# Kernel optimization log

Hardware: AMD Instinct MI355X
Metric: run time of the kernel (lower is better)

Reference implementation:

```python
import math
import jax, jax.numpy as jnp
import numpy as np

NUM_HEADS = 16
HEAD_DIM = 64
NB_FEATURES = 256
EPS = 1e-06
DATA_NORM = HEAD_DIM ** (-0.25)


def setup_inputs() -> dict:
    key = jax.random.key(0)
    ks = jax.random.split(key, 5)
    B, N, C = 4, 4096, 1024
    x = jax.random.normal(ks[0], (B, N, C), dtype=jnp.float32)
    w_qkv = jax.random.normal(ks[1], (C, 3 * C), dtype=jnp.float32) * (C ** -0.5)
    b_qkv = jnp.zeros((3 * C,), dtype=jnp.float32)
    w_out = jax.random.normal(ks[2], (C, C), dtype=jnp.float32) * (C ** -0.5)
    b_out = jnp.zeros((C,), dtype=jnp.float32)
    proj = jax.random.normal(ks[3], (NUM_HEADS, NB_FEATURES, HEAD_DIM), dtype=jnp.float32)
    proj = proj / jnp.linalg.norm(proj, axis=-1, keepdims=True)  # F.normalize(dim=-1)
    return {"x": x, "w_qkv": w_qkv, "b_qkv": b_qkv, "w_out": w_out, "b_out": b_out,
            "proj_matrix": proj}


def _feature_map(x, proj):
    # x: [b,h,n,d], proj: [h,m,d] -> [b,h,n,m]
    x = x * DATA_NORM
    x_proj = jnp.einsum('bhnd,hmd->bhnm', x, proj)
    sq_norms = 0.5 * jnp.sum(x * x, axis=-1, keepdims=True)
    x_proj = x_proj - sq_norms
    x_proj = x_proj - jnp.max(x_proj, axis=-1, keepdims=True)
    return (jnp.exp(x_proj) + EPS) / math.sqrt(NB_FEATURES)


def reference(x, w_qkv, b_qkv, w_out, b_out, proj_matrix):
    B, N, C = x.shape
    h, d = NUM_HEADS, HEAD_DIM
    qkv = x @ w_qkv + b_qkv                     # [B,N,3C]
    q, k, v = jnp.split(qkv, 3, axis=-1)
    to_heads = lambda z: z.reshape(B, N, h, d).transpose(0, 2, 1, 3)  # [B,h,N,d]
    q, k, v = to_heads(q), to_heads(k), to_heads(v)

    q_prime = _feature_map(q, proj_matrix)      # [B,h,N,m]
    k_prime = _feature_map(k, proj_matrix)      # [B,h,N,m]

    k_sum = jnp.sum(k_prime, axis=2)                          # [B,h,m]
    kv = jnp.einsum('bhnm,bhnd->bhmd', k_prime, v)            # [B,h,m,d]
    numerator = jnp.einsum('bhnm,bhmd->bhnd', q_prime, kv)    # [B,h,N,d]
    denominator = jnp.einsum('bhnm,bhm->bhn', q_prime, k_sum) + EPS
    out = numerator / denominator[..., None]

    out = out.transpose(0, 2, 1, 3).reshape(B, N, C)
    return out @ w_out + b_out
```

## Files before the change

### kernel.cpp

```cpp
#include <hip/hip_runtime.h>
#include <hip/hip_bf16.h>
#include <stdint.h>


#define DN 0.35355339059327379f
#define EPSF 1e-6f
#define INV_SQRT_M 0.0625f

typedef __attribute__((ext_vector_type(8))) short bf16x8;
typedef __attribute__((ext_vector_type(4))) float f32x4;

static __device__ __forceinline__ short f2bf(float f) {
    __hip_bfloat16 h = __float2bfloat16(f);
    return *(short*)&h;
}
static __device__ __forceinline__ void gload16(const void* g, void* l) {
    __builtin_amdgcn_global_load_lds(
        (const __attribute__((address_space(1))) void*)g,
        (__attribute__((address_space(3))) void*)l,
        16, 0, 0);
}

__global__ __launch_bounds__(256) void conv_x(const float* __restrict__ X,
                                              short* __restrict__ Xb) {
    int i = blockIdx.x * 256 + threadIdx.x;
    float4 v = ((const float4*)X)[i];
    short4 o;
    o.x = f2bf(v.x); o.y = f2bf(v.y); o.z = f2bf(v.z); o.w = f2bf(v.w);
    ((short4*)Xb)[i] = o;
}

__global__ __launch_bounds__(256) void convt_w(const float* __restrict__ W,
                                               short* __restrict__ WT,
                                               int K, int NN) {
    __shared__ short tile[64][66];
    int t = threadIdx.x;
    int k0 = blockIdx.y * 64, n0 = blockIdx.x * 64;
    for (int i = t; i < 4096; i += 256) {
        int r = i >> 6, c = i & 63;
        tile[r][c] = f2bf(W[(size_t)(k0 + r) * NN + n0 + c]);
    }
    __syncthreads();
    for (int i = t; i < 4096; i += 256) {
        int r = i >> 6, c = i & 63;
        WT[(size_t)(n0 + r) * K + k0 + c] = tile[c][r];
    }
}

__global__ __launch_bounds__(256) void conv_proj(const float* __restrict__ proj,
                                                 short* __restrict__ pjb) {
    int e = blockIdx.x * 256 + threadIdx.x;
    int m = (e >> 6) & 255, d = e & 63;
    int base = e & ~63;
    pjb[base + (d ^ ((m & 7) << 3))] = f2bf(proj[e]);
}

__device__ __forceinline__ void gemm_core128(const short* __restrict__ A,
                                             const short* __restrict__ BT,
                                             int rowBase, int colBase,
                                             char* smem, f32x4 acc[4][4]) {
    const int K = 1024;
    int t = threadIdx.x, lane = t & 63, w = t >> 6;
    int li = lane & 15, g = lane >> 4;
    int wm = w >> 1, wn = w & 1;

    const char* aSrc[4]; const char* bSrc[4]; int aOff[4];
#pragma unroll
    for (int c = 0; c < 4; ++c) {
        int idx = c * 256 + t;
        int r = idx >> 3, s = t & 7;
        aOff[c] = idx * 16;
        aSrc[c] = (const char*)(A + (size_t)(rowBase + r) * K + ((s ^ (r & 7)) * 8));
        bSrc[c] = (const char*)(BT + (size_t)(colBase + r) * K + ((s ^ (r & 7)) * 8));
    }
#pragma unroll
    for (int m = 0; m < 4; ++m)
#pragma unroll
        for (int n = 0; n < 4; ++n) acc[m][n] = (f32x4){0.f, 0.f, 0.f, 0.f};

#pragma unroll
    for (int c = 0; c < 4; ++c) {
        gload16(aSrc[c], smem + aOff[c]);
        gload16(bSrc[c], smem + 16384 + aOff[c]);
    }

    int swz = (li & 7) << 4;

    for (int tt = 0; tt < 16; ++tt) {
        int cur = tt & 1;
        if (tt < 15) {
            char* d = smem + (cur ^ 1) * 32768;
#pragma unroll
            for (int c = 0; c < 4; ++c) {
                gload16(aSrc[c] + (size_t)(tt + 1) * 128, d + aOff[c]);
                gload16(bSrc[c] + (size_t)(tt + 1) * 128, d + 16384 + aOff[c]);
            }
            asm volatile("s_waitcnt vmcnt(8)" ::: "memory");
        } else {
            asm volatile("s_waitcnt vmcnt(0)" ::: "memory");
        }
        __builtin_amdgcn_sched_barrier(0);
        __builtin_amdgcn_s_barrier();
        __builtin_amdgcn_sched_barrier(0);
        __builtin_amdgcn_s_setprio(1);
        const char* bA = smem + cur * 32768;
        const char* bB = bA + 16384;
#pragma unroll
        for (int ks = 0; ks < 2; ++ks) {
            int kb = ks * 64 + g * 16;
            bf16x8 af[4], bv[4];
#pragma unroll
            for (int m = 0; m < 4; ++m)
                af[m] = *(const bf16x8*)(bA + (wm * 64 + m * 16 + li) * 128 + (kb ^ swz));
#pragma unroll
            for (int n = 0; n < 4; ++n)
                bv[n] = *(const bf16x8*)(bB + (wn * 64 + n * 16 + li) * 128 + (kb ^ swz));
#pragma unroll
            for (int m = 0; m < 4; ++m)
#pragma unroll
                for (int n = 0; n < 4; ++n)
                    acc[m][n] = __builtin_amdgcn_mfma_f32_16x16x32_bf16(
                        af[m], bv[n], acc[m][n], 0, 0, 0);
        }
        __builtin_amdgcn_s_setprio(0);
        __builtin_amdgcn_sched_barrier(0);
        __builtin_amdgcn_s_barrier();
        __builtin_amdgcn_sched_barrier(0);
    }
}

__global__ __launch_bounds__(256, 2) void mfma_gemm_qkv(
        const short* __restrict__ A, const short* __restrict__ BT,
        const float* __restrict__ bias,
        short* __restrict__ Qh, short* __restrict__ Kh, short* __restrict__ Vt) {
    __shared__ __align__(16) char smem[65536];
    int t = threadIdx.x, lane = t & 63, w = t >> 6;
    int li = lane & 15, g = lane >> 4, wm = w >> 1, wn = w & 1;
    int lin = blockIdx.x;
    int bx = lin % 24, by = lin / 24;
    int rowBase = by * 128, colBase = bx * 128;

    f32x4 acc[4][4];
    gemm_core128(A, BT, rowBase, colBase, smem, acc);

    float bcol[4];
#pragma unroll
    for (int n = 0; n < 4; ++n) bcol[n] = bias[colBase + wn * 64 + n * 16 + li];
    int whichB = colBase >> 10;

    if (whichB == 2) {
#pragma unroll
        for (int n = 0; n < 4; ++n) {
            int gc = colBase + wn * 64 + n * 16 + li;
            int hh = (gc & 1023) >> 6, dd = gc & 63;
#pragma unroll
            for (int m = 0; m < 4; ++m) {
                int gr0 = rowBase + wm * 64 + m * 16 + g * 4;
                int b = gr0 >> 12, nn0 = gr0 & 4095;
                short4 o;
                o.x = f2bf(acc[m][n][0] + bcol[n]);
                o.y = f2bf(acc[m][n][1] + bcol[n]);
                o.z = f2bf(acc[m][n][2] + bcol[n]);
                o.w = f2bf(acc[m][n][3] + bcol[n]);
                int nsw = (nn0 & ~63) | ((nn0 & 63) ^ ((dd & 7) << 3));
                *(short4*)&Vt[((size_t)(b * 16 + hh) * 64 + dd) * 4096 + nsw] = o;
            }
        }
    } else {
        short* dst = (whichB == 0) ? Qh : Kh;
        int hh = ((colBase + wn * 64) & 1023) >> 6;
        float* wreg = (float*)(smem + w * 8704);
#pragma unroll
        for (int r = 0; r < 2; ++r) {
#pragma unroll
            for (int mi = 0; mi < 2; ++mi)
#pragma unroll
                for (int n = 0; n < 4; ++n)
#pragma unroll
                    for (int jj = 0; jj < 4; ++jj)
                        wreg[(mi * 16 + g * 4 + jj) * 68 + n * 16 + li] =
                            (acc[2 * r + mi][n][jj] + bcol[n]) * DN;
            int row = lane >> 1, h2 = lane & 1;
            int tok = rowBase + wm * 64 + r * 32 + row;
            int b = tok >> 12, nn = tok & 4095;
            size_t base = ((size_t)(b * 16 + hh) * 4096 + nn) * 64;
#pragma unroll
            for (int k = 0; k < 4; ++k) {
                float4 v0 = *(const float4*)&wreg[row * 68 + h2 * 32 + k * 8];
                float4 v1 = *(const float4*)&wreg[row * 68 + h2 * 32 + k * 8 + 4];
                bf16x8 ov;
                ov[0] = f2bf(v0.x); ov[1] = f2bf(v0.y);
                ov[2] = f2bf(v0.z); ov[3] = f2bf(v0.w);
                ov[4] = f2bf(v1.x); ov[5] = f2bf(v1.y);
                ov[6] = f2bf(v1.z); ov[7] = f2bf(v1.w);
                int dgrp = (h2 * 4 + k) ^ (tok & 7);
                *(bf16x8*)&dst[base + dgrp * 8] = ov;
            }
        }
    }
}

template<int Q, int S>
static __device__ __forceinline__ void phase_compute(
        const char* smem, int tt, int wm, int wn, int li, int g, int swz,
        f32x4 (&acc)[2][4][2][2]) {
    const char* bA = smem + ((tt & 1) << 16) + (Q << 14);
    const char* bB = smem + ((tt & 1) << 16) + 32768 + (S << 14);
    bf16x8 af[4][2], bf[2][2];
#pragma unroll
    for (int fr = 0; fr < 4; ++fr) {
        int row = wm * 64 + fr * 16 + li;
#pragma unroll
        for (int kk = 0; kk < 2; ++kk)
            af[fr][kk] = *(const bf16x8*)(bA + row * 128 + ((kk * 64 + g * 16) ^ swz));
    }
#pragma unroll
    for (int fn = 0; fn < 2; ++fn) {
        int row = wn * 32 + fn * 16 + li;
#pragma unroll
        for (int kk = 0; kk < 2; ++kk)
            bf[fn][kk] = *(const bf16x8*)(bB + row * 128 + ((kk * 64 + g * 16) ^ swz));
    }
    __builtin_amdgcn_s_setprio(1);
#pragma unroll
    for (int kk = 0; kk < 2; ++kk)
#pragma unroll
        for (int fr = 0; fr < 4; ++fr)
#pragma unroll
            for (int fn = 0; fn < 2; ++fn)
                acc[Q][fr][S][fn] = __builtin_amdgcn_mfma_f32_16x16x32_bf16(
                    af[fr][kk], bf[fn][kk], acc[Q][fr][S][fn], 0, 0, 0);
    __builtin_amdgcn_s_setprio(0);
}

static __device__ __forceinline__ void gemm_core256(const short* __restrict__ A,
                                                    const short* __restrict__ BT,
                                                    int rowBase, int colBase,
                                                    char* smem,
                                                    f32x4 (&acc)[2][4][2][2]) {
    const int K = 1024;
    int t = threadIdx.x, lane = t & 63;
    int li = lane & 15, g = lane >> 4;
    int w = t >> 6, wm = w >> 2, wn = w & 3;
    int swz = (li & 7) << 4;

    int idxA = t, idxB = 512 + t;
    int rA = idxA >> 3, sA = idxA & 7;
    int rB = idxB >> 3, sB = idxB & 7;
    const char* Ab = (const char*)(A + (size_t)rowBase * K);
    const char* Bb = (const char*)(BT + (size_t)colBase * K);
    int srcOffA = rA * 2048 + ((sA ^ (rA & 7)) * 16);
    int srcOffB = rB * 2048 + ((sB ^ (rB & 7)) * 16);
    int dstOffA = idxA * 16, dstOffB = idxB * 16;

#define STG(op_, half_, tile_) do {                                           \
    char* d_ = smem + (((tile_) & 1) << 16) + ((op_) << 15) + ((half_) << 14);\
    const char* s_ = ((op_) ? Bb : Ab) + (half_) * 262144 + (tile_) * 128;    \
    gload16(s_ + srcOffA, d_ + dstOffA);                                      \
    gload16(s_ + srcOffB, d_ + dstOffB);                                      \
} while (0)

#define PH(q_, s_, vm_, dost_, sop_, shalf_, stile_) do {                     \
    if (dost_) STG(sop_, shalf_, stile_);                                     \
    asm volatile("s_waitcnt vmcnt(" #vm_ ")" ::: "memory");                   \
    __builtin_amdgcn_sched_barrier(0);                                        \
    __builtin_amdgcn_s_barrier();                                             \
    __builtin_amdgcn_sched_barrier(0);                                        \
    phase_compute<q_, s_>(smem, tt, wm, wn, li, g, swz, acc);                 \
} while (0)

#pragma unroll
    for (int q = 0; q < 2; ++q)
#pragma unroll
        for (int fr = 0; fr < 4; ++fr)
#pragma unroll
            for (int s = 0; s < 2; ++s)
#pragma unroll
                for (int fn = 0; fn < 2; ++fn)
                    acc[q][fr][s][fn] = (f32x4){0.f, 0.f, 0.f, 0.f};

    STG(1, 0, 0);
    STG(0, 1, 0);
    STG(0, 0, 0);
    STG(1, 1, 0);
    STG(1, 0, 1);
    STG(0, 1, 1);

    for (int tt = 0; tt < 14; ++tt) {
        PH(0, 0,  8, true, 0, 0, tt + 1);
        PH(1, 0, 12, true, 1, 1, tt + 1);
        PH(1, 1, 10, true, 1, 0, tt + 2);
        PH(0, 1, 12, true, 0, 1, tt + 2);
    }
    {
        int tt = 14;
        PH(0, 0,  8, true, 0, 0, 15);
        PH(1, 0, 12, true, 1, 1, 15);
        PH(1, 1,  8, false, 0, 0, 0);
        PH(0, 1,  8, false, 0, 0, 0);
    }
    {
        int tt = 15;
        PH(0, 0, 2, false, 0, 0, 0);
        PH(1, 0, 4, false, 0, 0, 0);
        PH(1, 1, 0, false, 0, 0, 0);
        PH(0, 1, 0, false, 0, 0, 0);
    }
    __builtin_amdgcn_s_barrier();
#undef PH
#undef STG
}

__global__ __launch_bounds__(512) void mfma_gemm_out(
        const short* __restrict__ A, const short* __restrict__ BT,
        const float* __restrict__ bias, float* __restrict__ C) {
    __shared__ __align__(16) char smem[131072];
    int lin = blockIdx.x;
    int bx = lin & 3, by = lin >> 2;
    int rowBase = by * 256, colBase = bx * 256;

    f32x4 acc[2][4][2][2];
    gemm_core256(A, BT, rowBase, colBase, smem, acc);

    int t = threadIdx.x, lane = t & 63, w = t >> 6;
    int li = lane & 15, g = lane >> 4, wm = w >> 2, wn = w & 3;
    float bcol[2][2];
#pragma unroll
    for (int s = 0; s < 2; ++s)
#pragma unroll
        for (int fn = 0; fn < 2; ++fn)
            bcol[s][fn] = bias[colBase + s * 128 + wn * 32 + fn * 16 + li];

    float* wreg = (float*)(smem + w * 5632);
#pragma unroll
    for (int q = 0; q < 2; ++q)
#pragma unroll
        for (int fp = 0; fp < 2; ++fp)
#pragma unroll
            for (int s = 0; s < 2; ++s) {
#pragma unroll
                for (int fr2 = 0; fr2 < 2; ++fr2)
#pragma unroll
                    for (int fn = 0; fn < 2; ++fn)
#pragma unroll
                        for (int jj = 0; jj < 4; ++jj)
                            wreg[(fr2 * 16 + g * 4 + jj) * 44 + fn * 16 + li] =
                                acc[q][fp * 2 + fr2][s][fn][jj] + bcol[s][fn];
                int row2 = lane >> 1, hh2 = lane & 1;
                int gr = rowBase + q * 128 + wm * 64 + fp * 32 + row2;
                float* cp = C + (size_t)gr * 1024 + colBase + s * 128 + wn * 32 + hh2 * 16;
#pragma unroll
                for (int k = 0; k < 4; ++k)
                    *(float4*)&cp[k * 4] = *(const float4*)&wreg[row2 * 44 + hh2 * 16 + k * 4];
            }
}

__global__ __launch_bounds__(256) void fmap_mfma(const short* __restrict__ Kh,
                                                 const short* __restrict__ Vt,
                                                 const short* __restrict__ pjb,
                                                 float* __restrict__ kvpart,
                                                 float* __restrict__ kspart) {
    int bh = blockIdx.y, ch = blockIdx.x, h = bh & 15;
    int t = threadIdx.x, lane = t & 63, w = t >> 6;
    int g = lane >> 4, li = lane & 15;
    __shared__ __align__(16) short pj[256 * 64];
    __shared__ __align__(16) short kt[64 * 64];
    __shared__ __align__(16) short vt[64 * 64];
    __shared__ __align__(16) short Pl[4][64 * 40];
    __shared__ __align__(16) float maxw[4][64];

    const short* kbase = Kh + ((size_t)bh * 4096 + ch * 512) * 64;
    const short* vbase = Vt + (size_t)bh * 64 * 4096 + ch * 512;

    {
        const short* psrc = pjb + (size_t)h * 16384;
#pragma unroll
        for (int c2 = 0; c2 < 8; ++c2) {
            int c = 8 * w + c2;
            gload16(psrc + c * 512 + lane * 8, pj + c * 512);
        }
#pragma unroll
        for (int c2 = 0; c2 < 2; ++c2) {
            int c = 2 * w + c2;
            gload16(kbase + c * 512 + lane * 8, kt + c * 512);
            int d = 8 * c + (lane >> 3);
            gload16(vbase + (size_t)d * 4096 + (lane & 7) * 8, vt + c * 512);
        }
    }
    __syncthreads();

    f32x4 acc[4][4];
#pragma unroll
    for (int i = 0; i < 4; ++i)
#pragma unroll
        for (int j = 0; j < 4; ++j) acc[i][j] = (f32x4){0.f, 0.f, 0.f, 0.f};
    float ksacc[4] = {0.f, 0.f, 0.f, 0.f};

    int swz = (li & 7) << 4;

    for (int tile = 0; tile < 8; ++tile) {
        bf16x8 rk0, rk1, rv0, rv1;
        if (tile < 7) {
            int c0 = 2 * w, c1 = 2 * w + 1;
            size_t kof = (size_t)((tile + 1) * 64) * 64;
            rk0 = *(const bf16x8*)(kbase + kof + c0 * 512 + lane * 8);
            rk1 = *(const bf16x8*)(kbase + kof + c1 * 512 + lane * 8);
            int d0 = 8 * c0 + (lane >> 3), d1 = 8 * c1 + (lane >> 3);
            rv0 = *(const bf16x8*)(vbase + (size_t)d0 * 4096 + (tile + 1) * 64 + (lane & 7) * 8);
            rv1 = *(const bf16x8*)(vbase + (size_t)d1 * 4096 + (tile + 1) * 64 + (lane & 7) * 8);
        }

        f32x4 sacc[4][4];
#pragma unroll
        for (int i = 0; i < 4; ++i)
#pragma unroll
            for (int j = 0; j < 4; ++j) sacc[i][j] = (f32x4){0.f, 0.f, 0.f, 0.f};
#pragma unroll
        for (int ks = 0; ks < 2; ++ks) {
            int kb = ks * 64 + g * 16;
            bf16x8 afr[4], bfr[4];
#pragma unroll
            for (int ni = 0; ni < 4; ++ni)
                afr[ni] = *(const bf16x8*)((const char*)kt +
                           (16 * ni + li) * 128 + (kb ^ swz));
#pragma unroll
            for (int mi = 0; mi < 4; ++mi)
                bfr[mi] = *(const bf16x8*)((const char*)pj +
                           (64 * w + 16 * mi + li) * 128 + (kb ^ swz));
#pragma unroll
            for (int ni = 0; ni < 4; ++ni)
#pragma unroll
                for (int mi = 0; mi < 4; ++mi)
                    sacc[ni][mi] = __builtin_amdgcn_mfma_f32_16x16x32_bf16(
                        afr[ni], bfr[mi], sacc[ni][mi], 0, 0, 0);
        }

        float mxl[4][4];
#pragma unroll
        for (int ni = 0; ni < 4; ++ni)
#pragma unroll
            for (int jj = 0; jj < 4; ++jj) {
                float m0 = fmaxf(sacc[ni][0][jj], sacc[ni][1][jj]);
                float m1 = fmaxf(sacc[ni][2][jj], sacc[ni][3][jj]);
                mxl[ni][jj] = fmaxf(m0, m1);
            }
#pragma unroll
        for (int off = 1; off <= 8; off <<= 1)
#pragma unroll
            for (int ni = 0; ni < 4; ++ni)
#pragma unroll
                for (int jj = 0; jj < 4; ++jj)
                    mxl[ni][jj] = fmaxf(mxl[ni][jj], __shfl_xor(mxl[ni][jj], off));
        if (li == 0) {
#pragma unroll
            for (int ni = 0; ni < 4; ++ni)
                *(float4*)&maxw[w][16 * ni + 4 * g] =
                    make_float4(mxl[ni][0], mxl[ni][1], mxl[ni][2], mxl[ni][3]);
        }
        __syncthreads();

#pragma unroll
        for (int hf = 0; hf < 2; ++hf) {
#pragma unroll
            for (int ni2 = 0; ni2 < 2; ++ni2) {
                int ni = 2 * hf + ni2;
                float4 a0 = *(const float4*)&maxw[0][16 * ni + 4 * g];
                float4 a1 = *(const float4*)&maxw[1][16 * ni + 4 * g];
                float4 a2 = *(const float4*)&maxw[2][16 * ni + 4 * g];
                float4 a3 = *(const float4*)&maxw[3][16 * ni + 4 * g];
                float mm[4];
                mm[0] = fmaxf(fmaxf(a0.x, a1.x), fmaxf(a2.x, a3.x));
                mm[1] = fmaxf(fmaxf(a0.y, a1.y), fmaxf(a2.y, a3.y));
                mm[2] = fmaxf(fmaxf(a0.z, a1.z), fmaxf(a2.z, a3.z));
                mm[3] = fmaxf(fmaxf(a0.w, a1.w), fmaxf(a2.w, a3.w));
#pragma unroll
                for (int mi = 0; mi < 4; ++mi) {
                    float p0 = (__expf(sacc[ni][mi][0] - mm[0]) + EPSF) * INV_SQRT_M;
                    float p1 = (__expf(sacc[ni][mi][1] - mm[1]) + EPSF) * INV_SQRT_M;
                    float p2 = (__expf(sacc[ni][mi][2] - mm[2]) + EPSF) * INV_SQRT_M;
                    float p3 = (__expf(sacc[ni][mi][3] - mm[3]) + EPSF) * INV_SQRT_M;
                    ksacc[mi] += (p0 + p1) + (p2 + p3);
                    uint32_t u0 = (uint32_t)(uint16_t)f2bf(p0) |
                                  ((uint32_t)(uint16_t)f2bf(p1) << 16);
                    uint32_t u1 = (uint32_t)(uint16_t)f2bf(p2) |
                                  ((uint32_t)(uint16_t)f2bf(p3) << 16);
                    int m_l = 16 * mi + li;
                    *(uint2*)((char*)Pl[w] + m_l * 80 + 32 * ni2 + 8 * g) =
                        make_uint2(u0, u1);
                }
            }
#pragma unroll
            for (int mi = 0; mi < 4; ++mi) {
                bf16x8 pa = *(const bf16x8*)((const char*)Pl[w] +
                             (16 * mi + li) * 80 + 16 * g);
#pragma unroll
                for (int di = 0; di < 4; ++di) {
                    bf16x8 bv = *(const bf16x8*)((const char*)vt +
                                 (16 * di + li) * 128 + ((64 * hf + 16 * g) ^ swz));
                    acc[mi][di] = __builtin_amdgcn_mfma_f32_16x16x32_bf16(
                        pa, bv, acc[mi][di], 0, 0, 0);
                }
            }
        }
        __syncthreads();
        if (tile < 7) {
            int c0 = 2 * w, c1 = 2 * w + 1;
            *(bf16x8*)((char*)kt + c0 * 1024 + lane * 16) = rk0;
            *(bf16x8*)((char*)kt + c1 * 1024 + lane * 16) = rk1;
            *(bf16x8*)((char*)vt + c0 * 1024 + lane * 16) = rv0;
            *(bf16x8*)((char*)vt + c1 * 1024 + lane * 16) = rv1;
            __syncthreads();
        }
    }

#pragma unroll
    for (int mi = 0; mi < 4; ++mi) {
        ksacc[mi] += __shfl_xor(ksacc[mi], 16);
        ksacc[mi] += __shfl_xor(ksacc[mi], 32);
    }
    if (lane < 16) {
#pragma unroll
        for (int mi = 0; mi < 4; ++mi)
            kspart[(bh * 8 + ch) * 256 + 64 * w + 16 * mi + li] = ksacc[mi];
    }
    float* kvb = kvpart + (size_t)(bh * 8 + ch) * 16384;
#pragma unroll
    for (int mi = 0; mi < 4; ++mi)
#pragma unroll
        for (int di = 0; di < 4; ++di) {
            int d = 16 * di + li, m0 = 64 * w + 16 * mi + 4 * g;
            *(float4*)&kvb[d * 256 + m0] =
                make_float4(acc[mi][di][0], acc[mi][di][1],
                            acc[mi][di][2], acc[mi][di][3]);
        }
}

__global__ __launch_bounds__(256) void reduce_kv(const float* __restrict__ kvpart,
                                                 const float* __restrict__ kspart,
                                                 short* __restrict__ kvsT) {
    int bh = blockIdx.y, bx = blockIdx.x, t = threadIdx.x;
    if (bx < 4) {
#pragma unroll
        for (int i = 0; i < 16; ++i) {
            int idx = t + i * 256;
            int d = 16 * bx + (idx >> 8), m = idx & 255;
            float s = 0.f;
            size_t base = ((size_t)(bh * 8) * 64 + d) * 256 + m;
#pragma unroll
            for (int c = 0; c < 8; ++c) s += kvpart[base + (size_t)c * 16384];
            int widx = (m & 128) + ((m & 127) ^ ((d & 7) << 3));
            kvsT[((size_t)bh * 80 + d) * 256 + widx] = f2bf(s);
        }
    } else {
        float s = 0.f;
#pragma unroll
        for (int c = 0; c < 8; ++c) s += kspart[((bh * 8 + c) << 8) + t];
        kvsT[((size_t)bh * 80 + 64) * 256 + t] = f2bf(s);
        for (int i = t; i < 15 * 256; i += 256) {
            int r = 65 + (i >> 8), cc = i & 255;
            kvsT[((size_t)bh * 80 + r) * 256 + cc] = 0;
        }
    }
}

__global__ __launch_bounds__(256) void contract_mfma(
        const short* __restrict__ Qh,
        const short* __restrict__ pjb,
        const short* __restrict__ kvsT,
        short* __restrict__ attn) {
    int bh = blockIdx.y, rb = blockIdx.x, h = bh & 15, b = bh >> 4;
    int t = threadIdx.x, lane = t & 63, w = t >> 6;
    __shared__ __align__(16) short qs[128 * 64];
    __shared__ __align__(16) short pj[128 * 64];
    __shared__ __align__(16) short Pl[64 * 128];
    __shared__ __align__(16) short kvl[80 * 128];

    {
        const short* src = Qh + ((size_t)bh * 4096 + rb * 128) * 64;
#pragma unroll
        for (int c2 = 0; c2 < 4; ++c2) {
            int c = 4 * w + c2;
            gload16(src + (c * 8 + (lane >> 3)) * 64 + (lane & 7) * 8,
                    qs + c * 512);
        }
    }

    f32x4 acc5[2][5];
#pragma unroll
    for (int rg = 0; rg < 2; ++rg)
#pragma unroll
        for (int i = 0; i < 5; ++i) acc5[rg][i] = (f32x4){0.f, 0.f, 0.f, 0.f};

    int g = lane >> 4, li = lane & 15;

    for (int half = 0; half < 2; ++half) {
        const short* psrc = pjb + (size_t)h * 16384 + half * 8192;
#pragma unroll
        for (int c2 = 0; c2 < 4; ++c2) {
            int c = 4 * w + c2;
            gload16(psrc + (c * 8 + (lane >> 3)) * 64 + (lane & 7) * 8,
                    pj + c * 512);
        }
        const short* ksrc = kvsT + (size_t)bh * 80 * 256 + half * 128;
#pragma unroll
        for (int c2 = 0; c2 < 5; ++c2) {
            int c = 5 * w + c2;
            gload16(ksrc + (c * 4 + (lane >> 4)) * 256 + (lane & 15) * 8,
                    kvl + c * 512);
        }
        __syncthreads();

#pragma unroll
        for (int rg = 0; rg < 2; ++rg) {
            f32x4 sacc[2][4];
#pragma unroll
            for (int mi = 0; mi < 2; ++mi)
#pragma unroll
                for (int ni = 0; ni < 4; ++ni) sacc[mi][ni] = (f32x4){0.f, 0.f, 0.f, 0.f};
#pragma unroll
            for (int ks = 0; ks < 2; ++ks) {
                int kbyte = ks * 64 + g * 16;
                bf16x8 afr[2], bfr[4];
#pragma unroll
                for (int mi = 0; mi < 2; ++mi) {
                    int mr = 32 * w + 16 * mi + li;
                    afr[mi] = *(const bf16x8*)((const char*)pj +
                               mr * 128 + (kbyte ^ ((mr & 7) << 4)));
                }
#pragma unroll
                for (int ni = 0; ni < 4; ++ni) {
                    int qr = rg * 64 + 16 * ni + li;
                    bfr[ni] = *(const bf16x8*)((const char*)qs +
                               qr * 128 + (kbyte ^ ((qr & 7) << 4)));
                }
#pragma unroll
                for (int mi = 0; mi < 2; ++mi)
#pragma unroll
                    for (int ni = 0; ni < 4; ++ni)
                        sacc[mi][ni] = __builtin_amdgcn_mfma_f32_16x16x32_bf16(
                            afr[mi], bfr[ni], sacc[mi][ni], 0, 0, 0);
            }

#pragma unroll
            for (int mi = 0; mi < 2; ++mi) {
                int m0 = 32 * w + 16 * mi + 4 * g;
#pragma unroll
                for (int ni = 0; ni < 4; ++ni) {
                    int row = 16 * ni + li;
                    float e0 = (__expf(sacc[mi][ni][0]) + EPSF) * INV_SQRT_M;
                    float e1 = (__expf(sacc[mi][ni][1]) + EPSF) * INV_SQRT_M;
                    float e2 = (__expf(sacc[mi][ni][2]) + EPSF) * INV_SQRT_M;
                    float e3 = (__expf(sacc[mi][ni][3]) + EPSF) * INV_SQRT_M;
                    uint32_t u0 = (uint32_t)(uint16_t)f2bf(e0) |
                                  ((uint32_t)(uint16_t)f2bf(e1) << 16);
                    uint32_t u1 = (uint32_t)(uint16_t)f2bf(e2) |
                                  ((uint32_t)(uint16_t)f2bf(e3) << 16);
                    int byte = row * 256 + ((m0 * 2) ^ ((row & 7) << 4));
                    *(uint2*)((char*)Pl + byte) = make_uint2(u0, u1);
                }
            }
            __syncthreads();

            int rowA = 16 * w + li;
            int abase = rowA * 256;
            int asw = (rowA & 7) << 4;
#pragma unroll
            for (int ks = 0; ks < 4; ++ks) {
                int kbyte = ks * 64 + g * 16;
                bf16x8 pa = *(const bf16x8*)((const char*)Pl + abase + (kbyte ^ asw));
#pragma unroll
                for (int ni = 0; ni < 5; ++ni) {
                    int rowB = 16 * ni + li;
                    bf16x8 bv = *(const bf16x8*)((const char*)kvl +
                                 rowB * 256 + (kbyte ^ ((rowB & 7) << 4)));
                    acc5[rg][ni] = __builtin_amdgcn_mfma_f32_16x16x32_bf16(
                        pa, bv, acc5[rg][ni], 0, 0, 0);
                }
            }
            __syncthreads();
        }
    }

#pragma unroll
    for (int rg = 0; rg < 2; ++rg) {
        float dj[4];
#pragma unroll
        for (int jj = 0; jj < 4; ++jj)
            dj[jj] = __shfl(acc5[rg][4][jj], lane & 48) + EPSF;
#pragma unroll
        for (int ni = 0; ni < 4; ++ni) {
            int d = 16 * ni + li;
#pragma unroll
            for (int jj = 0; jj < 4; ++jj) {
                int n = rb * 128 + rg * 64 + 16 * w + 4 * g + jj;
                attn[((size_t)b * 4096 + n) * 1024 + h * 64 + d] =
                    f2bf(acc5[rg][ni][jj] / dj[jj]);
            }
        }
    }
}

extern "C" void kernel_launch(void* const* d_in, const int* in_sizes, int n_in,
                              void* d_out, int out_size, void* d_ws, size_t ws_size,
                              hipStream_t stream) {
    const float* x      = (const float*)d_in[0];
    const float* w_qkv  = (const float*)d_in[1];
    const float* b_qkv  = (const float*)d_in[2];
    const float* w_out  = (const float*)d_in[3];
    const float* b_out  = (const float*)d_in[4];
    const float* proj   = (const float*)d_in[5];
    float* out = (float*)d_out;

    char* w = (char*)d_ws;
    short* xb     = (short*)(w);
    short* wqT    = (short*)(w + 33554432);
    short* wOT    = (short*)(w + 39845888);
    short* Qh     = (short*)(w + 41943040);
    short* Kh     = (short*)(w + 75497472);
    short* Vt     = (short*)(w + 109051904);
    float* kvpart = (float*)(w);
    float* kspart = (float*)(w + 142606336);
    short* kvsT   = (short*)(w + 143130624);
    short* pjb    = (short*)(w + 145752064);
    short* attn   = Kh;

    conv_x<<<dim3(16384), 256, 0, stream>>>(x, xb);
    convt_w<<<dim3(48, 16), 256, 0, stream>>>(w_qkv, wqT, 1024, 3072);
    convt_w<<<dim3(16, 16), 256, 0, stream>>>(w_out, wOT, 1024, 1024);
    conv_proj<<<dim3(1024), 256, 0, stream>>>(proj, pjb);
    mfma_gemm_qkv<<<dim3(3072), 256, 0, stream>>>(xb, wqT, b_qkv, Qh, Kh, Vt);
    fmap_mfma<<<dim3(8, 64), 256, 0, stream>>>(Kh, Vt, pjb, kvpart, kspart);
    reduce_kv<<<dim3(5, 64), 256, 0, stream>>>(kvpart, kspart, kvsT);
    contract_mfma<<<dim3(32, 64), 256, 0, stream>>>(Qh, pjb, kvsT, attn);
    mfma_gemm_out<<<dim3(256), 512, 0, stream>>>(attn, wOT, b_out, out);
}
```

Measured before the change: 308.6 us.

## Merge prep conversion kernels into one launch and keep projection fragments in registers

Folds the four input-conversion kernels (x to bf16, both weight transposes, projection swizzle) into one kernel that branches on block index, cutting three launches and the gaps between them. In fmap_mfma and contract_mfma the projection matrix is no longer staged in shared memory. Each wave loads its fixed projection MFMA fragments straight from global memory into registers once and reuses them across tiles. This drops shared-memory traffic and LDS footprint, which may raise occupancy, but it adds register pressure and uncoalesced fragment loads.

New measurement: 298.6 us. -3.2%, faster.

```diff
diff --git a/kernel.cpp b/kernel.cpp
--- a/kernel.cpp
+++ b/kernel.cpp
@@ -21,38 +21,54 @@
         16, 0, 0);
 }
 
-__global__ __launch_bounds__(256) void conv_x(const float* __restrict__ X,
-                                              short* __restrict__ Xb) {
-    int i = blockIdx.x * 256 + threadIdx.x;
-    float4 v = ((const float4*)X)[i];
-    short4 o;
-    o.x = f2bf(v.x); o.y = f2bf(v.y); o.z = f2bf(v.z); o.w = f2bf(v.w);
-    ((short4*)Xb)[i] = o;
-}
-
-__global__ __launch_bounds__(256) void convt_w(const float* __restrict__ W,
-                                               short* __restrict__ WT,
-                                               int K, int NN) {
+__global__ __launch_bounds__(256) void prep(const float* __restrict__ X,
+                                            short* __restrict__ Xb,
+                                            const float* __restrict__ Wq,
+                                            short* __restrict__ WqT,
+                                            const float* __restrict__ Wo,
+                                            short* __restrict__ WoT,
+                                            const float* __restrict__ proj,
+                                            short* __restrict__ pjb) {
     __shared__ short tile[64][66];
-    int t = threadIdx.x;
-    int k0 = blockIdx.y * 64, n0 = blockIdx.x * 64;
-    for (int i = t; i < 4096; i += 256) {
-        int r = i >> 6, c = i & 63;
-        tile[r][c] = f2bf(W[(size_t)(k0 + r) * NN + n0 + c]);
-    }
-    __syncthreads();
-    for (int i = t; i < 4096; i += 256) {
-        int r = i >> 6, c = i & 63;
-        WT[(size_t)(n0 + r) * K + k0 + c] = tile[c][r];
-    }
-}
-
-__global__ __launch_bounds__(256) void conv_proj(const float* __restrict__ proj,
-                                                 short* __restrict__ pjb) {
-    int e = blockIdx.x * 256 + threadIdx.x;
-    int m = (e >> 6) & 255, d = e & 63;
-    int base = e & ~63;
-    pjb[base + (d ^ ((m & 7) << 3))] = f2bf(proj[e]);
+    int b = blockIdx.x, t = threadIdx.x;
+    if (b < 16384) {
+        int i = b * 256 + t;
+        float4 v = ((const float4*)X)[i];
+        short4 o;
+        o.x = f2bf(v.x); o.y = f2bf(v.y); o.z = f2bf(v.z); o.w = f2bf(v.w);
+        ((short4*)Xb)[i] = o;
+    } else if (b < 17152) {
+        int idx = b - 16384;
+        int k0 = (idx / 48) * 64, n0 = (idx % 48) * 64;
+        const int K = 1024, NN = 3072;
+        for (int i = t; i < 4096; i += 256) {
+            int r = i >> 6, c = i & 63;
+            tile[r][c] = f2bf(Wq[(size_t)(k0 + r) * NN + n0 + c]);
+        }
+        __syncthreads();
+        for (int i = t; i < 4096; i += 256) {
+            int r = i >> 6, c = i & 63;
+            WqT[(size_t)(n0 + r) * K + k0 + c] = tile[c][r];
+        }
+    } else if (b < 17408) {
+        int idx = b - 17152;
+        int k0 = (idx / 16) * 64, n0 = (idx % 16) * 64;
+        const int K = 1024, NN = 1024;
+        for (int i = t; i < 4096; i += 256) {
+            int r = i >> 6, c = i & 63;
+            tile[r][c] = f2bf(Wo[(size_t)(k0 + r) * NN + n0 + c]);
+        }
+        __syncthreads();
+        for (int i = t; i < 4096; i += 256) {
+            int r = i >> 6, c = i & 63;
+            WoT[(size_t)(n0 + r) * K + k0 + c] = tile[c][r];
+        }
+    } else {
+        int e = (b - 17408) * 256 + t;
+        int m = (e >> 6) & 255, d = e & 63;
+        int base = e & ~63;
+        pjb[base + (d ^ ((m & 7) << 3))] = f2bf(proj[e]);
+    }
 }
 
 __device__ __forceinline__ void gemm_core128(const short* __restrict__ A,
@@ -363,7 +379,6 @@
     int bh = blockIdx.y, ch = blockIdx.x, h = bh & 15;
     int t = threadIdx.x, lane = t & 63, w = t >> 6;
     int g = lane >> 4, li = lane & 15;
-    __shared__ __align__(16) short pj[256 * 64];
     __shared__ __align__(16) short kt[64 * 64];
     __shared__ __align__(16) short vt[64 * 64];
     __shared__ __align__(16) short Pl[4][64 * 40];
@@ -371,14 +386,20 @@
 
     const short* kbase = Kh + ((size_t)bh * 4096 + ch * 512) * 64;
     const short* vbase = Vt + (size_t)bh * 64 * 4096 + ch * 512;
-
+    int swz = (li & 7) << 4;
+
+    bf16x8 pjf[2][4];
     {
-        const short* psrc = pjb + (size_t)h * 16384;
-#pragma unroll
-        for (int c2 = 0; c2 < 8; ++c2) {
-            int c = 8 * w + c2;
-            gload16(psrc + c * 512 + lane * 8, pj + c * 512);
-        }
+        const char* ph = (const char*)(pjb + (size_t)h * 16384);
+#pragma unroll
+        for (int ks = 0; ks < 2; ++ks)
+#pragma unroll
+            for (int mi = 0; mi < 4; ++mi)
+                pjf[ks][mi] = *(const bf16x8*)(ph +
+                    (64 * w + 16 * mi + li) * 128 + ((ks * 64 + g * 16) ^ swz));
+    }
+
+    {
 #pragma unroll
         for (int c2 = 0; c2 < 2; ++c2) {
             int c = 2 * w + c2;
@@ -395,8 +416,6 @@
 #pragma unroll
         for (int j = 0; j < 4; ++j) acc[i][j] = (f32x4){0.f, 0.f, 0.f, 0.f};
     float ksacc[4] = {0.f, 0.f, 0.f, 0.f};
-
-    int swz = (li & 7) << 4;
 
     for (int tile = 0; tile < 8; ++tile) {
         bf16x8 rk0, rk1, rv0, rv1;
@@ -418,21 +437,17 @@
 #pragma unroll
         for (int ks = 0; ks < 2; ++ks) {
             int kb = ks * 64 + g * 16;
-            bf16x8 afr[4], bfr[4];
+            bf16x8 afr[4];
 #pragma unroll
             for (int ni = 0; ni < 4; ++ni)
                 afr[ni] = *(const bf16x8*)((const char*)kt +
                            (16 * ni + li) * 128 + (kb ^ swz));
 #pragma unroll
-            for (int mi = 0; mi < 4; ++mi)
-                bfr[mi] = *(const bf16x8*)((const char*)pj +
-                           (64 * w + 16 * mi + li) * 128 + (kb ^ swz));
-#pragma unroll
             for (int ni = 0; ni < 4; ++ni)
 #pragma unroll
                 for (int mi = 0; mi < 4; ++mi)
                     sacc[ni][mi] = __builtin_amdgcn_mfma_f32_16x16x32_bf16(
-                        afr[ni], bfr[mi], sacc[ni][mi], 0, 0, 0);
+                        afr[ni], pjf[ks][mi], sacc[ni][mi], 0, 0, 0);
         }
 
         float mxl[4][4];
@@ -571,7 +586,6 @@
     int bh = blockIdx.y, rb = blockIdx.x, h = bh & 15, b = bh >> 4;
     int t = threadIdx.x, lane = t & 63, w = t >> 6;
     __shared__ __align__(16) short qs[128 * 64];
-    __shared__ __align__(16) short pj[128 * 64];
     __shared__ __align__(16) short Pl[64 * 128];
     __shared__ __align__(16) short kvl[80 * 128];
 
@@ -594,12 +608,17 @@
     int g = lane >> 4, li = lane & 15;
 
     for (int half = 0; half < 2; ++half) {
-        const short* psrc = pjb + (size_t)h * 16384 + half * 8192;
-#pragma unroll
-        for (int c2 = 0; c2 < 4; ++c2) {
-            int c = 4 * w + c2;
-            gload16(psrc + (c * 8 + (lane >> 3)) * 64 + (lane & 7) * 8,
-                    pj + c * 512);
+        bf16x8 pjf[2][2];
+        {
+            const char* ph = (const char*)(pjb + (size_t)h * 16384 + half * 8192);
+#pragma unroll
+            for (int ks = 0; ks < 2; ++ks)
+#pragma unroll
+                for (int mi = 0; mi < 2; ++mi) {
+                    int mr = 32 * w + 16 * mi + li;
+                    pjf[ks][mi] = *(const bf16x8*)(ph +
+                        mr * 128 + ((ks * 64 + g * 16) ^ ((mr & 7) << 4)));
+                }
         }
         const short* ksrc = kvsT + (size_t)bh * 80 * 256 + half * 128;
 #pragma unroll
@@ -620,13 +639,7 @@
 #pragma unroll
             for (int ks = 0; ks < 2; ++ks) {
                 int kbyte = ks * 64 + g * 16;
-                bf16x8 afr[2], bfr[4];
-#pragma unroll
-                for (int mi = 0; mi < 2; ++mi) {
-                    int mr = 32 * w + 16 * mi + li;
-                    afr[mi] = *(const bf16x8*)((const char*)pj +
-                               mr * 128 + (kbyte ^ ((mr & 7) << 4)));
-                }
+                bf16x8 bfr[4];
 #pragma unroll
                 for (int ni = 0; ni < 4; ++ni) {
                     int qr = rg * 64 + 16 * ni + li;
@@ -638,7 +651,7 @@
 #pragma unroll
                     for (int ni = 0; ni < 4; ++ni)
                         sacc[mi][ni] = __builtin_amdgcn_mfma_f32_16x16x32_bf16(
-                            afr[mi], bfr[ni], sacc[mi][ni], 0, 0, 0);
+                            pjf[ks][mi], bfr[ni], sacc[mi][ni], 0, 0, 0);
             }
 
 #pragma unroll
@@ -724,10 +737,7 @@
     short* pjb    = (short*)(w + 145752064);
     short* attn   = Kh;
 
-    conv_x<<<dim3(16384), 256, 0, stream>>>(x, xb);
-    convt_w<<<dim3(48, 16), 256, 0, stream>>>(w_qkv, wqT, 1024, 3072);
-    convt_w<<<dim3(16, 16), 256, 0, stream>>>(w_out, wOT, 1024, 1024);
-    conv_proj<<<dim3(1024), 256, 0, stream>>>(proj, pjb);
+    prep<<<dim3(18432), 256, 0, stream>>>(x, xb, w_qkv, wqT, w_out, wOT, proj, pjb);
     mfma_gemm_qkv<<<dim3(3072), 256, 0, stream>>>(xb, wqT, b_qkv, Qh, Kh, Vt);
     fmap_mfma<<<dim3(8, 64), 256, 0, stream>>>(Kh, Vt, pjb, kvpart, kspart);
     reduce_kv<<<dim3(5, 64), 256, 0, stream>>>(kvpart, kspart, kvsT);
```
